# Performance work log

Hardware: AMD Instinct MI355X
Metric: run time of the kernel (lower is better)

The kernel has to match this reference:

```python
import jax, jax.numpy as jnp
import numpy as np

B, C, H, W = 2, 512, 128, 128
L_NUM, HEADS, LEVELS, POINTS = 6, 8, 1, 4
HEAD_DIM = C // HEADS


def setup_inputs() -> dict:
    key = jax.random.key(0)
    ks = jax.random.split(key, 16)
    s = 0.02
    rn = lambda k, shape, scale=s: jax.random.normal(k, shape, jnp.float32) * scale
    return dict(
        bev_feat=jax.random.normal(ks[0], (B, C, H, W), jnp.float32),
        lidar_feat=jax.random.normal(ks[1], (B, C, H, W), jnp.float32),
        Wv=rn(ks[2], (L_NUM, C, C)), bv=jnp.zeros((L_NUM, C), jnp.float32),
        Woff=rn(ks[3], (L_NUM, C, HEADS * LEVELS * POINTS * 2)),
        boff=rn(ks[4], (L_NUM, HEADS * LEVELS * POINTS * 2), 0.5),
        Waw=rn(ks[5], (L_NUM, C, HEADS * LEVELS * POINTS)),
        baw=jnp.zeros((L_NUM, HEADS * LEVELS * POINTS), jnp.float32),
        Wout=rn(ks[6], (L_NUM, C, C)), bout=jnp.zeros((L_NUM, C), jnp.float32),
        ln1_g=jnp.ones((L_NUM, C), jnp.float32), ln1_b=jnp.zeros((L_NUM, C), jnp.float32),
        W1=rn(ks[7], (L_NUM, C, C)), W2=rn(ks[8], (L_NUM, C, C)),
        ln2_g=jnp.ones((L_NUM, C), jnp.float32), ln2_b=jnp.zeros((L_NUM, C), jnp.float32),
        pe_W1=rn(ks[9], (2, C), 0.5),
        pe_bn_g=jnp.ones((C,), jnp.float32), pe_bn_b=jnp.zeros((C,), jnp.float32),
        pe_bn_m=jnp.zeros((C,), jnp.float32), pe_bn_v=jnp.ones((C,), jnp.float32),
        pe_W2=rn(ks[10], (C, C)),
    )


def _layer_norm(x, g, b):
    mu = jnp.mean(x, -1, keepdims=True)
    var = jnp.mean((x - mu) ** 2, -1, keepdims=True)
    return (x - mu) * jax.lax.rsqrt(var + 1e-5) * g + b


def _bilinear_gather(v_flat, locx, locy):
    # v_flat: (B, heads, H*W, d); locx/locy: (B, heads, S) normalized [0,1]
    # grid_sample semantics: align_corners=False, zero padding
    x = locx * W - 0.5
    y = locy * H - 0.5
    x0f = jnp.floor(x); y0f = jnp.floor(y)
    wx = x - x0f; wy = y - y0f
    x0 = x0f.astype(jnp.int32); y0 = y0f.astype(jnp.int32)

    def corner(xi, yi, w):
        inb = (xi >= 0) & (xi < W) & (yi >= 0) & (yi < H)
        idx = jnp.clip(yi, 0, H - 1) * W + jnp.clip(xi, 0, W - 1)
        g = jnp.take_along_axis(v_flat, idx[..., None], axis=2)
        return g * (w * inb)[..., None]

    return (corner(x0, y0, (1 - wx) * (1 - wy)) + corner(x0 + 1, y0, wx * (1 - wy))
            + corner(x0, y0 + 1, (1 - wx) * wy) + corner(x0 + 1, y0 + 1, wx * wy))


def reference(bev_feat, lidar_feat, Wv, bv, Woff, boff, Waw, baw, Wout, bout,
              ln1_g, ln1_b, W1, W2, ln2_g, ln2_b,
              pe_W1, pe_bn_g, pe_bn_b, pe_bn_m, pe_bn_v, pe_W2):
    N = H * W
    # sparse voxelization: keep rows with all-nonzero features, pack valid-first per batch
    lf = jnp.transpose(lidar_feat, (0, 2, 3, 1)).reshape(B, N, C)
    mask = jnp.all(lf != 0, axis=-1)                       # (B,N)
    order = jnp.argsort((~mask).astype(jnp.int32), axis=1, stable=True)  # valid first
    valid = jnp.take_along_axis(mask, order, axis=1)       # (B,N)
    q = jnp.take_along_axis(lf, order[..., None], axis=1) * valid[..., None]
    hh = jnp.arange(N) // W
    ww = jnp.arange(N) % W
    ref_all = jnp.stack([ww / W, hh / H], -1).astype(jnp.float32)  # (N,2) = (x,y)
    ref = jnp.broadcast_to(ref_all, (B, N, 2))
    ref = jnp.take_along_axis(ref, order[..., None], axis=1) * valid[..., None]
    # learned positional embedding (BatchNorm in eval mode)
    pe = ref.reshape(B * N, 2) @ pe_W1
    pe = (pe - pe_bn_m) * jax.lax.rsqrt(pe_bn_v + 1e-5) * pe_bn_g + pe_bn_b
    q_pos = (jax.nn.relu(pe) @ pe_W2).reshape(B, N, C)
    feat_flat = jnp.transpose(bev_feat.reshape(B, C, N), (0, 2, 1))  # (B,N,C)
    norm_xy = jnp.array([W, H], jnp.float32)  # offset normalizer per level (w,h)
    for i in range(L_NUM):
        ident = q
        x = q + q_pos
        v = (feat_flat @ Wv[i] + bv[i]).reshape(B, N, HEADS, HEAD_DIM)
        v_flat = jnp.transpose(v, (0, 2, 1, 3))  # (B,heads,N,d)
        off = (x @ Woff[i] + boff[i]).reshape(B, N, HEADS, LEVELS * POINTS, 2)
        aw = jax.nn.softmax((x @ Waw[i] + baw[i]).reshape(B, N, HEADS, LEVELS * POINTS), axis=-1)
        loc = ref[:, :, None, None, :] + off / norm_xy      # (B,N,heads,P,2)
        locx = jnp.transpose(loc[..., 0], (0, 2, 1, 3)).reshape(B, HEADS, N * POINTS)
        locy = jnp.transpose(loc[..., 1], (0, 2, 1, 3)).reshape(B, HEADS, N * POINTS)
        samp = _bilinear_gather(v_flat, locx, locy).reshape(B, HEADS, N, POINTS, HEAD_DIM)
        awt = jnp.transpose(aw, (0, 2, 1, 3))               # (B,heads,N,P)
        out = jnp.sum(samp * awt[..., None], axis=3)        # (B,heads,N,d)
        out = jnp.transpose(out, (0, 2, 1, 3)).reshape(B, N, C)
        q = out @ Wout[i] + bout[i] + ident                 # dropout in eval = identity
        q = _layer_norm(q, ln1_g[i], ln1_b[i])
        q = jax.nn.relu(q @ W1[i]) @ W2[i] + q
        q = _layer_norm(q, ln2_g[i], ln2_b[i])
    # scatter back to dense (B,C,H,W); invalid voxels stay zero
    slots = jnp.zeros((B, N, C), q.dtype)
    slots = slots.at[jnp.arange(B)[:, None], order].set(q * valid[..., None])
    return jnp.transpose(slots.reshape(B, H, W, C), (0, 3, 1, 2))
```

## Files before the change

### kernel.cpp

```cpp
#include <hip/hip_runtime.h>
#include <cstdint>
#include <cstddef>

#define BDIM 2
#define CDIM 512
#define HDIM 128
#define WDIM 128
#define NDIM (HDIM * WDIM)
#define LNUM 6
#define NHEADS 8
#define HEAD_DIM 64
#define NPTS 4
#define BN_TOT (BDIM * NDIM)

typedef unsigned short u16;
typedef __attribute__((ext_vector_type(8))) short bf16x8;
typedef __attribute__((ext_vector_type(4))) float f32x4;

__device__ __forceinline__ u16 f2bf(float x) {
    unsigned u = __float_as_uint(x);
    u += 0x7fffu + ((u >> 16) & 1u);
    return (u16)(u >> 16);
}
__device__ __forceinline__ float bf2f(u16 h) {
    return __uint_as_float(((unsigned)h) << 16);
}

__device__ __forceinline__ void load_lds16(const void* g, void* l) {
    __builtin_amdgcn_global_load_lds(
        (const __attribute__((address_space(1))) void*)g,
        (__attribute__((address_space(3))) void*)l, 16, 0, 0);
}

__global__ void mask_kernel(const float* __restrict__ lidar, int* __restrict__ mask)
{
    int idx = blockIdx.x * blockDim.x + threadIdx.x;
    if (idx >= BN_TOT) return;
    int b = idx / NDIM;
    int n = idx - b * NDIM;
    const float* p = lidar + (size_t)b * CDIM * NDIM + n;
    int ok = 1;
#pragma unroll 8
    for (int c = 0; c < CDIM; ++c)
        ok &= (p[(size_t)c * NDIM] != 0.0f);
    mask[idx] = ok;
}

__global__ void order_kernel(const int* __restrict__ mask, int* __restrict__ order,
                             int* __restrict__ nvalid)
{
    int b = blockIdx.x;
    const int* m = mask + b * NDIM;
    int* ord = order + b * NDIM;
    __shared__ int part[256];
    __shared__ int totalValid;
    int t = threadIdx.x;
    const int CHUNK = NDIM / 256;
    int base = t * CHUNK;
    int cnt = 0;
    for (int i = 0; i < CHUNK; ++i) cnt += m[base + i];
    part[t] = cnt;
    __syncthreads();
    for (int s = 1; s < 256; s <<= 1) {
        int v = (t >= s) ? part[t - s] : 0;
        __syncthreads();
        part[t] += v;
        __syncthreads();
    }
    if (t == 255) { totalValid = part[255]; nvalid[b] = part[255]; }
    __syncthreads();
    int validBefore = (t == 0) ? 0 : part[t - 1];
    int nv = totalValid;
    for (int i = 0; i < CHUNK; ++i) {
        int n = base + i;
        if (m[n]) { ord[validBefore] = n; validBefore++; }
        else      { int invBefore = n - validBefore; ord[nv + invBefore] = n; }
    }
}

__global__ void ref_kernel(const int* __restrict__ order, const int* __restrict__ nvalid,
                           float* __restrict__ ref)
{
    int idx = blockIdx.x * blockDim.x + threadIdx.x;
    if (idx >= BN_TOT) return;
    int b = idx / NDIM;
    int j = idx - b * NDIM;
    int n = order[idx];
    float flag = (j < nvalid[b]) ? 1.0f : 0.0f;
    int hh = n / WDIM;
    int ww = n - hh * WDIM;
    ref[(size_t)idx * 2 + 0] = ((float)ww / (float)WDIM) * flag;
    ref[(size_t)idx * 2 + 1] = ((float)hh / (float)HDIM) * flag;
}

__global__ void pack_q_kernel(const float* __restrict__ lidar, const int* __restrict__ order,
                              const int* __restrict__ nvalid, u16* __restrict__ q)
{
    __shared__ float tile[32][33];
    __shared__ int ord_s[32];
    int b  = blockIdx.z;
    int j0 = blockIdx.x * 32;
    int c0 = blockIdx.y * 32;
    int tx = threadIdx.x, ty = threadIdx.y;
    if (ty == 0) ord_s[tx] = order[b * NDIM + j0 + tx];
    __syncthreads();
    const float* src = lidar + (size_t)b * CDIM * NDIM;
#pragma unroll
    for (int k = 0; k < 4; ++k) {
        int cl = ty * 4 + k;
        tile[cl][tx] = src[(size_t)(c0 + cl) * NDIM + ord_s[tx]];
    }
    __syncthreads();
    int nv = nvalid[b];
#pragma unroll
    for (int k = 0; k < 4; ++k) {
        int jl = ty * 4 + k;
        int j = j0 + jl;
        float f = (j < nv) ? 1.0f : 0.0f;
        q[((size_t)b * NDIM + j) * CDIM + c0 + tx] = f2bf(tile[tx][jl] * f);
    }
}

__global__ void scatter_kernel(const u16* __restrict__ q, const int* __restrict__ order,
                               const int* __restrict__ nvalid, float* __restrict__ out)
{
    __shared__ float tile[32][33];
    __shared__ int ord_s[32];
    int b  = blockIdx.z;
    int j0 = blockIdx.x * 32;
    int c0 = blockIdx.y * 32;
    int tx = threadIdx.x, ty = threadIdx.y;
    if (ty == 0) ord_s[tx] = order[b * NDIM + j0 + tx];
    __syncthreads();
    int nv = nvalid[b];
#pragma unroll
    for (int k = 0; k < 4; ++k) {
        int jl = ty * 4 + k;
        int j = j0 + jl;
        float f = (j < nv) ? 1.0f : 0.0f;
        tile[jl][tx] = bf2f(q[((size_t)b * NDIM + j) * CDIM + c0 + tx]) * f;
    }
    __syncthreads();
    float* dst = out + (size_t)b * CDIM * NDIM;
#pragma unroll
    for (int k = 0; k < 4; ++k) {
        int cl = ty * 4 + k;
        dst[(size_t)(c0 + cl) * NDIM + ord_s[tx]] = tile[tx][cl];
    }
}

__global__ void tconv_kernel(const float* __restrict__ src, u16* __restrict__ dst)
{
    __shared__ float t[32][33];
    int k0 = blockIdx.x * 32, n0 = blockIdx.y * 32;
    int tx = threadIdx.x, ty = threadIdx.y;
#pragma unroll
    for (int j = 0; j < 4; ++j) {
        int kl = ty * 4 + j;
        t[kl][tx] = src[(size_t)(k0 + kl) * 512 + n0 + tx];
    }
    __syncthreads();
#pragma unroll
    for (int j = 0; j < 4; ++j) {
        int nl = ty * 4 + j;
        dst[(size_t)(n0 + nl) * 512 + k0 + tx] = f2bf(t[tx][nl]);
    }
}

__global__ void tconv_offaw_kernel(const float* __restrict__ woff,
                                   const float* __restrict__ waw,
                                   u16* __restrict__ dst)
{
    __shared__ float t[32][33];
    int k0 = blockIdx.x * 32, n0 = blockIdx.y * 32;
    int tx = threadIdx.x, ty = threadIdx.y;
#pragma unroll
    for (int j = 0; j < 4; ++j) {
        int kl = ty * 4 + j;
        int n = n0 + tx;
        float v = (n < 64) ? woff[(size_t)(k0 + kl) * 64 + n]
                           : waw[(size_t)(k0 + kl) * 32 + (n - 64)];
        t[kl][tx] = v;
    }
    __syncthreads();
#pragma unroll
    for (int j = 0; j < 4; ++j) {
        int nl = ty * 4 + j;
        dst[(size_t)(n0 + nl) * 512 + k0 + tx] = f2bf(t[tx][nl]);
    }
}

__global__ void bev_conv_kernel(const float* __restrict__ bev, u16* __restrict__ dst)
{
    __shared__ float t[32][33];
    int b  = blockIdx.z;
    int n0 = blockIdx.x * 32;
    int c0 = blockIdx.y * 32;
    int tx = threadIdx.x, ty = threadIdx.y;
    const float* src = bev + (size_t)b * CDIM * NDIM;
#pragma unroll
    for (int j = 0; j < 4; ++j) {
        int cl = ty * 4 + j;
        t[cl][tx] = src[(size_t)(c0 + cl) * NDIM + n0 + tx];
    }
    __syncthreads();
#pragma unroll
    for (int j = 0; j < 4; ++j) {
        int nl = ty * 4 + j;
        dst[((size_t)b * NDIM + n0 + nl) * CDIM + c0 + tx] = f2bf(t[tx][nl]);
    }
}

__global__ void pe_hidden_kernel(const float* __restrict__ ref, const float* __restrict__ W1,
                                 const float* __restrict__ g, const float* __restrict__ bb,
                                 const float* __restrict__ m, const float* __restrict__ v,
                                 u16* __restrict__ out)
{
    int row = blockIdx.x;
    float r0 = ref[(size_t)row * 2 + 0];
    float r1 = ref[(size_t)row * 2 + 1];
    for (int c = threadIdx.x; c < CDIM; c += blockDim.x) {
        float pe = r0 * W1[c] + r1 * W1[CDIM + c];
        pe = (pe - m[c]) * rsqrtf(v[c] + 1e-5f) * g[c] + bb[c];
        out[(size_t)row * CDIM + c] = f2bf(fmaxf(pe, 0.0f));
    }
}

__global__ void add_bf_kernel(const u16* __restrict__ q, const u16* __restrict__ qpos,
                              u16* __restrict__ x)
{
    size_t i = (size_t)blockIdx.x * blockDim.x + threadIdx.x;
    uint4 qa = ((const uint4*)q)[i];
    uint4 pv = ((const uint4*)qpos)[i];
    unsigned qw[4] = {qa.x, qa.y, qa.z, qa.w};
    unsigned pw[4] = {pv.x, pv.y, pv.z, pv.w};
    unsigned rw[4];
#pragma unroll
    for (int k = 0; k < 4; ++k) {
        float a0 = bf2f((u16)(qw[k] & 0xffff)), a1 = bf2f((u16)(qw[k] >> 16));
        float p0 = bf2f((u16)(pw[k] & 0xffff)), p1 = bf2f((u16)(pw[k] >> 16));
        rw[k] = (unsigned)f2bf(a0 + p0) | ((unsigned)f2bf(a1 + p1) << 16);
    }
    uint4 r; r.x = rw[0]; r.y = rw[1]; r.z = rw[2]; r.w = rw[3];
    ((uint4*)x)[i] = r;
}

__global__ __launch_bounds__(256) void gemm_bf16(
    const u16* __restrict__ A, const u16* __restrict__ Bt,
    const float* __restrict__ bias, u16* __restrict__ outB, int relu)
{
    __shared__ u16 As[128 * 32];
    __shared__ u16 Bs[128 * 32];
    int tid = threadIdx.x;
    int wave = tid >> 6, lane = tid & 63;
    int wr = wave >> 1, wc = wave & 1;
    int quad = lane >> 4, l15 = lane & 15;
    int bm = blockIdx.y * 128, bn = blockIdx.x * 128;

    f32x4 acc[4][4];
#pragma unroll
    for (int i = 0; i < 4; ++i)
#pragma unroll
        for (int j = 0; j < 4; ++j) { f32x4 z = {0.f, 0.f, 0.f, 0.f}; acc[i][j] = z; }

    int e0 = wave * 512 + lane * 8;
    int e1 = (wave + 4) * 512 + lane * 8;
    const u16* Ag0 = A + (size_t)(bm + (e0 >> 5)) * 512 + (e0 & 31);
    const u16* Ag1 = A + (size_t)(bm + (e1 >> 5)) * 512 + (e1 & 31);
    const u16* Bg0 = Bt + (size_t)(bn + (e0 >> 5)) * 512 + (e0 & 31);
    const u16* Bg1 = Bt + (size_t)(bn + (e1 >> 5)) * 512 + (e1 & 31);

    for (int k0 = 0; k0 < 512; k0 += 32) {
        load_lds16(Ag0 + k0, &As[wave * 512]);
        load_lds16(Ag1 + k0, &As[(wave + 4) * 512]);
        load_lds16(Bg0 + k0, &Bs[wave * 512]);
        load_lds16(Bg1 + k0, &Bs[(wave + 4) * 512]);
        __syncthreads();
        bf16x8 av[4], bv[4];
#pragma unroll
        for (int mi = 0; mi < 4; ++mi)
            av[mi] = *(const bf16x8*)&As[(wr * 64 + mi * 16 + l15) * 32 + quad * 8];
#pragma unroll
        for (int ni = 0; ni < 4; ++ni)
            bv[ni] = *(const bf16x8*)&Bs[(wc * 64 + ni * 16 + l15) * 32 + quad * 8];
#pragma unroll
        for (int mi = 0; mi < 4; ++mi)
#pragma unroll
            for (int ni = 0; ni < 4; ++ni)
                acc[mi][ni] = __builtin_amdgcn_mfma_f32_16x16x32_bf16(
                    av[mi], bv[ni], acc[mi][ni], 0, 0, 0);
        __syncthreads();
    }

    int rowb = bm + wr * 64;
    int colb = bn + wc * 64;
#pragma unroll
    for (int mi = 0; mi < 4; ++mi) {
#pragma unroll
        for (int ni = 0; ni < 4; ++ni) {
            int col = colb + ni * 16 + l15;
            float bi = bias ? bias[col] : 0.0f;
#pragma unroll
            for (int r = 0; r < 4; ++r) {
                int row = rowb + mi * 16 + quad * 4 + r;
                float val = acc[mi][ni][r] + bi;
                if (relu) val = fmaxf(val, 0.0f);
                outB[(size_t)row * 512 + col] = f2bf(val);
            }
        }
    }
}

__global__ __launch_bounds__(512, 4) void gemm_ln(
    const u16* __restrict__ A, const u16* __restrict__ Bt,
    const float* __restrict__ bias, const u16* __restrict__ resid,
    const float* __restrict__ g, const float* __restrict__ bta,
    u16* __restrict__ outQ, const u16* __restrict__ qpos, u16* __restrict__ outX)
{
    __shared__ u16 As[64 * 32];
    __shared__ u16 Bs[512 * 32];
    __shared__ float rs[8][64];
    __shared__ float rq[8][64];
    __shared__ float muL[64], invL[64];

    int tid = threadIdx.x;
    int wv = tid >> 6, lane = tid & 63;
    int quad = lane >> 4, l15 = lane & 15;
    int bm = blockIdx.x * 64;

    f32x4 acc[4][4];
#pragma unroll
    for (int i = 0; i < 4; ++i)
#pragma unroll
        for (int j = 0; j < 4; ++j) { f32x4 z = {0.f, 0.f, 0.f, 0.f}; acc[i][j] = z; }

    const u16* Ag = A + (size_t)(bm + wv * 16 + (lane >> 2)) * 512 + (lane & 3) * 8;
    u16* Al = As + wv * 512;
    const u16* Bg[4];
    u16* Bl[4];
#pragma unroll
    for (int it = 0; it < 4; ++it) {
        int s = wv * 4 + it;
        Bg[it] = Bt + (size_t)(s * 16 + (lane >> 2)) * 512 + (lane & 3) * 8;
        Bl[it] = Bs + s * 512;
    }

    for (int k0 = 0; k0 < 512; k0 += 32) {
        if (wv < 4) load_lds16(Ag + k0, Al);
#pragma unroll
        for (int it = 0; it < 4; ++it) load_lds16(Bg[it] + k0, Bl[it]);
        __syncthreads();
        bf16x8 av[4], bv[4];
#pragma unroll
        for (int mi = 0; mi < 4; ++mi)
            av[mi] = *(const bf16x8*)&As[(mi * 16 + l15) * 32 + quad * 8];
#pragma unroll
        for (int ni = 0; ni < 4; ++ni)
            bv[ni] = *(const bf16x8*)&Bs[(wv * 64 + ni * 16 + l15) * 32 + quad * 8];
#pragma unroll
        for (int mi = 0; mi < 4; ++mi)
#pragma unroll
            for (int ni = 0; ni < 4; ++ni)
                acc[mi][ni] = __builtin_amdgcn_mfma_f32_16x16x32_bf16(
                    av[mi], bv[ni], acc[mi][ni], 0, 0, 0);
        __syncthreads();
    }

    int colb = wv * 64;
    float biasv[4], gv[4], btv[4];
#pragma unroll
    for (int ni = 0; ni < 4; ++ni) {
        int c = colb + ni * 16 + l15;
        biasv[ni] = bias ? bias[c] : 0.0f;
        gv[ni] = g[c];
        btv[ni] = bta[c];
    }
#pragma unroll
    for (int mi = 0; mi < 4; ++mi) {
#pragma unroll
        for (int r = 0; r < 4; ++r) {
            size_t rowoff = (size_t)(bm + mi * 16 + quad * 4 + r) * 512;
#pragma unroll
            for (int ni = 0; ni < 4; ++ni) {
                int col = colb + ni * 16 + l15;
                acc[mi][ni][r] += biasv[ni] + bf2f(resid[rowoff + col]);
            }
        }
    }
#pragma unroll
    for (int mi = 0; mi < 4; ++mi) {
#pragma unroll
        for (int r = 0; r < 4; ++r) {
            float s = acc[mi][0][r] + acc[mi][1][r] + acc[mi][2][r] + acc[mi][3][r];
            float s2 = acc[mi][0][r] * acc[mi][0][r] + acc[mi][1][r] * acc[mi][1][r]
                     + acc[mi][2][r] * acc[mi][2][r] + acc[mi][3][r] * acc[mi][3][r];
#pragma unroll
            for (int m = 1; m < 16; m <<= 1) {
                s  += __shfl_xor(s, m, 64);
                s2 += __shfl_xor(s2, m, 64);
            }
            if (l15 == 0) {
                rs[wv][mi * 16 + quad * 4 + r] = s;
                rq[wv][mi * 16 + quad * 4 + r] = s2;
            }
        }
    }
    __syncthreads();
    if (tid < 64) {
        float s = 0.f, s2 = 0.f;
#pragma unroll
        for (int w = 0; w < 8; ++w) { s += rs[w][tid]; s2 += rq[w][tid]; }
        float mu = s * (1.0f / 512.0f);
        float var = s2 * (1.0f / 512.0f) - mu * mu;
        muL[tid] = mu;
        invL[tid] = rsqrtf(var + 1e-5f);
    }
    __syncthreads();
#pragma unroll
    for (int mi = 0; mi < 4; ++mi) {
#pragma unroll
        for (int r = 0; r < 4; ++r) {
            int lrow = mi * 16 + quad * 4 + r;
            float mu = muL[lrow], iv = invL[lrow];
            size_t rowoff = (size_t)(bm + lrow) * 512;
#pragma unroll
            for (int ni = 0; ni < 4; ++ni) {
                int col = colb + ni * 16 + l15;
                float y = (acc[mi][ni][r] - mu) * iv * gv[ni] + btv[ni];
                outQ[rowoff + col] = f2bf(y);
                if (outX)
                    outX[rowoff + col] = f2bf(y + bf2f(qpos[rowoff + col]));
            }
        }
    }
}

__global__ __launch_bounds__(256) void gemm_offaw(
    const u16* __restrict__ A, const u16* __restrict__ Bt,
    const float* __restrict__ boff, const float* __restrict__ baw,
    u16* __restrict__ offb, u16* __restrict__ awb)
{
    __shared__ u16 As[128 * 32];
    __shared__ u16 Bs[128 * 32];
    int tid = threadIdx.x;
    int wave = tid >> 6, lane = tid & 63;
    int wr = wave >> 1, wc = wave & 1;
    int quad = lane >> 4, l15 = lane & 15;
    int bm = blockIdx.y * 128;

    f32x4 acc[4][4];
#pragma unroll
    for (int i = 0; i < 4; ++i)
#pragma unroll
        for (int j = 0; j < 4; ++j) { f32x4 z = {0.f, 0.f, 0.f, 0.f}; acc[i][j] = z; }

    int e0 = wave * 512 + lane * 8;
    int e1 = (wave + 4) * 512 + lane * 8;
    int br0 = e0 >> 5; if (br0 > 95) br0 = 95;
    int br1 = e1 >> 5; if (br1 > 95) br1 = 95;
    const u16* Ag0 = A + (size_t)(bm + (e0 >> 5)) * 512 + (e0 & 31);
    const u16* Ag1 = A + (size_t)(bm + (e1 >> 5)) * 512 + (e1 & 31);
    const u16* Bg0 = Bt + (size_t)br0 * 512 + (e0 & 31);
    const u16* Bg1 = Bt + (size_t)br1 * 512 + (e1 & 31);

    for (int k0 = 0; k0 < 512; k0 += 32) {
        load_lds16(Ag0 + k0, &As[wave * 512]);
        load_lds16(Ag1 + k0, &As[(wave + 4) * 512]);
        load_lds16(Bg0 + k0, &Bs[wave * 512]);
        load_lds16(Bg1 + k0, &Bs[(wave + 4) * 512]);
        __syncthreads();
        bf16x8 av[4], bv[4];
#pragma unroll
        for (int mi = 0; mi < 4; ++mi)
            av[mi] = *(const bf16x8*)&As[(wr * 64 + mi * 16 + l15) * 32 + quad * 8];
#pragma unroll
        for (int ni = 0; ni < 4; ++ni)
            bv[ni] = *(const bf16x8*)&Bs[(wc * 64 + ni * 16 + l15) * 32 + quad * 8];
#pragma unroll
        for (int mi = 0; mi < 4; ++mi)
#pragma unroll
            for (int ni = 0; ni < 4; ++ni)
                acc[mi][ni] = __builtin_amdgcn_mfma_f32_16x16x32_bf16(
                    av[mi], bv[ni], acc[mi][ni], 0, 0, 0);
        __syncthreads();
    }

    int rowb = bm + wr * 64;
#pragma unroll
    for (int mi = 0; mi < 4; ++mi) {
#pragma unroll
        for (int ni = 0; ni < 4; ++ni) {
            int col = wc * 64 + ni * 16 + l15;
            if (col < 96) {
                float bi = (col < 64) ? boff[col] : baw[col - 64];
#pragma unroll
                for (int r = 0; r < 4; ++r) {
                    int row = rowb + mi * 16 + quad * 4 + r;
                    float val = acc[mi][ni][r] + bi;
                    if (col < 64) offb[(size_t)row * 64 + col] = f2bf(val);
                    else          awb[(size_t)row * 32 + (col - 64)] = f2bf(val);
                }
            }
        }
    }
}

__global__ __launch_bounds__(256) void sample_kernel(
    const float* __restrict__ ref, const u16* __restrict__ off,
    const u16* __restrict__ aw, const u16* __restrict__ v,
    u16* __restrict__ out)
{
    int bj = blockIdx.x * 4 + (threadIdx.x >> 6);
    int lane = threadIdx.x & 63;
    int h  = lane >> 3;
    int d8 = (lane & 7) * 8;
    int b  = bj >> 14;

    float rx = ref[(size_t)bj * 2 + 0];
    float ry = ref[(size_t)bj * 2 + 1];
    uint4 offv = *(const uint4*)(off + (size_t)bj * 64 + h * 8);
    uint2 awv  = *(const uint2*)(aw + (size_t)bj * 32 + h * 4);

    float l0 = bf2f((u16)(awv.x & 0xffff)), l1 = bf2f((u16)(awv.x >> 16));
    float l2 = bf2f((u16)(awv.y & 0xffff)), l3 = bf2f((u16)(awv.y >> 16));
    float mx = fmaxf(fmaxf(l0, l1), fmaxf(l2, l3));
    float e[4];
    e[0] = expf(l0 - mx); e[1] = expf(l1 - mx);
    e[2] = expf(l2 - mx); e[3] = expf(l3 - mx);
    float inv_es = 1.0f / (e[0] + e[1] + e[2] + e[3]);

    const u16* vb = v + (size_t)b * NDIM * CDIM + h * HEAD_DIM + d8;
    float acc[8] = {0.f, 0.f, 0.f, 0.f, 0.f, 0.f, 0.f, 0.f};
    unsigned ow[4] = {offv.x, offv.y, offv.z, offv.w};

#pragma unroll
    for (int p = 0; p < NPTS; ++p) {
        float ox = bf2f((u16)(ow[p] & 0xffff));
        float oy = bf2f((u16)(ow[p] >> 16));
        float X = rx * (float)WDIM + ox - 0.5f;
        float Y = ry * (float)HDIM + oy - 0.5f;
        float x0f = floorf(X), y0f = floorf(Y);
        float wx = X - x0f, wy = Y - y0f;
        int x0 = (int)x0f, y0 = (int)y0f;
        float ep = e[p];
#pragma unroll
        for (int cy = 0; cy < 2; ++cy) {
            int yy = y0 + cy;
            float wyc = cy ? wy : (1.0f - wy);
            int yin = (yy >= 0) & (yy < HDIM);
            int yc = min(max(yy, 0), HDIM - 1);
#pragma unroll
            for (int cx = 0; cx < 2; ++cx) {
                int xx = x0 + cx;
                float wxc = cx ? wx : (1.0f - wx);
                int xin = (xx >= 0) & (xx < WDIM);
                int xc = min(max(xx, 0), WDIM - 1);
                float wgt = ep * wyc * wxc * (float)(yin & xin);
                uint4 vv = *(const uint4*)(vb + (size_t)(yc * WDIM + xc) * CDIM);
                acc[0] += wgt * bf2f((u16)(vv.x & 0xffff));
                acc[1] += wgt * bf2f((u16)(vv.x >> 16));
                acc[2] += wgt * bf2f((u16)(vv.y & 0xffff));
                acc[3] += wgt * bf2f((u16)(vv.y >> 16));
                acc[4] += wgt * bf2f((u16)(vv.z & 0xffff));
                acc[5] += wgt * bf2f((u16)(vv.z >> 16));
                acc[6] += wgt * bf2f((u16)(vv.w & 0xffff));
                acc[7] += wgt * bf2f((u16)(vv.w >> 16));
            }
        }
    }
    uint4 r;
    r.x = (unsigned)f2bf(acc[0] * inv_es) | ((unsigned)f2bf(acc[1] * inv_es) << 16);
    r.y = (unsigned)f2bf(acc[2] * inv_es) | ((unsigned)f2bf(acc[3] * inv_es) << 16);
    r.z = (unsigned)f2bf(acc[4] * inv_es) | ((unsigned)f2bf(acc[5] * inv_es) << 16);
    r.w = (unsigned)f2bf(acc[6] * inv_es) | ((unsigned)f2bf(acc[7] * inv_es) << 16);
    *(uint4*)(out + (size_t)bj * CDIM + h * HEAD_DIM + d8) = r;
}

extern "C" void kernel_launch(void* const* d_in, const int* in_sizes, int n_in,
                              void* d_out, int out_size, void* d_ws, size_t ws_size,
                              hipStream_t stream)
{
    const float* bev   = (const float*)d_in[0];
    const float* lidar = (const float*)d_in[1];
    const float* Wv    = (const float*)d_in[2];
    const float* bv    = (const float*)d_in[3];
    const float* Woff  = (const float*)d_in[4];
    const float* boff  = (const float*)d_in[5];
    const float* Waw   = (const float*)d_in[6];
    const float* baw   = (const float*)d_in[7];
    const float* Wout  = (const float*)d_in[8];
    const float* bout  = (const float*)d_in[9];
    const float* ln1g  = (const float*)d_in[10];
    const float* ln1b  = (const float*)d_in[11];
    const float* W1    = (const float*)d_in[12];
    const float* W2    = (const float*)d_in[13];
    const float* ln2g  = (const float*)d_in[14];
    const float* ln2b  = (const float*)d_in[15];
    const float* peW1  = (const float*)d_in[16];
    const float* peg   = (const float*)d_in[17];
    const float* peb   = (const float*)d_in[18];
    const float* pem   = (const float*)d_in[19];
    const float* pev   = (const float*)d_in[20];
    const float* pevW2 = (const float*)d_in[21];

    const size_t NC = (size_t)BN_TOT * CDIM;

    char* base = (char*)d_ws;
    u16* q      = (u16*)base;
    u16* actX   = (u16*)(base + NC * 2);
    u16* actA   = (u16*)(base + NC * 4);
    u16* actB   = (u16*)(base + NC * 6);
    u16* wt     = (u16*)(base + NC * 8);
    u16* offawt = wt + 4 * 512 * 512;
    u16* offb   = offawt + 96 * 512;
    u16* awb    = offb + (size_t)BN_TOT * 64;
    float* refb = (float*)(awb + (size_t)BN_TOT * 32);
    int* mask   = (int*)(refb + (size_t)BN_TOT * 2);
    int* order  = mask + BN_TOT;
    int* nvalid = order + BN_TOT;

    u16* qpos_bf = (u16*)d_out;
    u16* featT   = (u16*)d_out + NC;

    dim3 blk328(32, 8);
    dim3 gemm_grid(4, 256);
    dim3 offaw_grid(1, 256);
    int  ln_grid = BN_TOT / 64;

    mask_kernel<<<BN_TOT / 256, 256, 0, stream>>>(lidar, mask);
    order_kernel<<<BDIM, 256, 0, stream>>>(mask, order, nvalid);
    ref_kernel<<<BN_TOT / 256, 256, 0, stream>>>(order, nvalid, refb);
    pack_q_kernel<<<dim3(NDIM / 32, CDIM / 32, BDIM), blk328, 0, stream>>>(lidar, order, nvalid, q);
    bev_conv_kernel<<<dim3(NDIM / 32, CDIM / 32, BDIM), blk328, 0, stream>>>(bev, featT);

    pe_hidden_kernel<<<BN_TOT, 128, 0, stream>>>(refb, peW1, peg, peb, pem, pev, actA);
    tconv_kernel<<<dim3(16, 16), blk328, 0, stream>>>(pevW2, wt);
    gemm_bf16<<<gemm_grid, 256, 0, stream>>>(actA, wt, nullptr, qpos_bf, 0);

    add_bf_kernel<<<(unsigned)(NC / 8 / 256), 256, 0, stream>>>(q, qpos_bf, actX);

    for (int i = 0; i < LNUM; ++i) {
        const size_t WO = (size_t)i * CDIM * CDIM;
        tconv_kernel<<<dim3(16, 16), blk328, 0, stream>>>(Wv + WO,   wt + 0 * 262144);
        tconv_kernel<<<dim3(16, 16), blk328, 0, stream>>>(Wout + WO, wt + 1 * 262144);
        tconv_kernel<<<dim3(16, 16), blk328, 0, stream>>>(W1 + WO,   wt + 2 * 262144);
        tconv_kernel<<<dim3(16, 16), blk328, 0, stream>>>(W2 + WO,   wt + 3 * 262144);
        tconv_offaw_kernel<<<dim3(16, 3), blk328, 0, stream>>>(
            Woff + (size_t)i * CDIM * 64, Waw + (size_t)i * CDIM * 32, offawt);

        gemm_offaw<<<offaw_grid, 256, 0, stream>>>(actX, offawt,
                                                   boff + i * 64, baw + i * 32, offb, awb);
        gemm_bf16<<<gemm_grid, 256, 0, stream>>>(featT, wt + 0 * 262144, bv + i * CDIM,
                                                 actA, 0);
        sample_kernel<<<BN_TOT / 4, 256, 0, stream>>>(refb, offb, awb, actA, actB);
        gemm_ln<<<ln_grid, 512, 0, stream>>>(actB, wt + 1 * 262144, bout + i * CDIM,
                                             q, ln1g + i * CDIM, ln1b + i * CDIM,
                                             q, nullptr, nullptr);
        gemm_bf16<<<gemm_grid, 256, 0, stream>>>(q, wt + 2 * 262144, nullptr, actA, 1);
        gemm_ln<<<ln_grid, 512, 0, stream>>>(actA, wt + 3 * 262144, nullptr,
                                             q, ln2g + i * CDIM, ln2b + i * CDIM,
                                             q, qpos_bf,
                                             (i < LNUM - 1) ? actX : nullptr);
    }

    scatter_kernel<<<dim3(NDIM / 32, CDIM / 32, BDIM), blk328, 0, stream>>>(
        q, order, nvalid, (float*)d_out);
}
```

Before: 1.959 ms.

## Double-buffer LDS in GEMMs and batch weight transposes up front

Gives the three GEMM kernels double-buffered LDS tiles, so the load of the next K-slice is issued before computing on the current one, with one barrier per iteration instead of two. All per-layer weight transpose/convert launches are replaced by a few batched launches (grid z over layers) before the loop, storing every layer's bf16 weights separately. The actX buffer is dropped and actB reused for x. This hides global-load latency and removes about 30 small launches, at the cost of doubled LDS use per block, which can lower occupancy in gemm_ln.

```diff
diff --git a/kernel.cpp b/kernel.cpp
--- a/kernel.cpp
+++ b/kernel.cpp
@@ -149,9 +149,12 @@
     }
 }
 
-__global__ void tconv_kernel(const float* __restrict__ src, u16* __restrict__ dst)
+__global__ void tconv_b_kernel(const float* __restrict__ src0, u16* __restrict__ dst0)
 {
     __shared__ float t[32][33];
+    int z = blockIdx.z;
+    const float* src = src0 + (size_t)z * 512 * 512;
+    u16* dst = dst0 + (size_t)z * 512 * 512;
     int k0 = blockIdx.x * 32, n0 = blockIdx.y * 32;
     int tx = threadIdx.x, ty = threadIdx.y;
 #pragma unroll
@@ -167,11 +170,15 @@
     }
 }
 
-__global__ void tconv_offaw_kernel(const float* __restrict__ woff,
-                                   const float* __restrict__ waw,
-                                   u16* __restrict__ dst)
+__global__ void tconv_offaw_b_kernel(const float* __restrict__ woff0,
+                                     const float* __restrict__ waw0,
+                                     u16* __restrict__ dst0)
 {
     __shared__ float t[32][33];
+    int z = blockIdx.z;
+    const float* woff = woff0 + (size_t)z * 512 * 64;
+    const float* waw  = waw0 + (size_t)z * 512 * 32;
+    u16* dst = dst0 + (size_t)z * 96 * 512;
     int k0 = blockIdx.x * 32, n0 = blockIdx.y * 32;
     int tx = threadIdx.x, ty = threadIdx.y;
 #pragma unroll
@@ -249,8 +256,8 @@
     const u16* __restrict__ A, const u16* __restrict__ Bt,
     const float* __restrict__ bias, u16* __restrict__ outB, int relu)
 {
-    __shared__ u16 As[128 * 32];
-    __shared__ u16 Bs[128 * 32];
+    __shared__ u16 As[2][128 * 32];
+    __shared__ u16 Bs[2][128 * 32];
     int tid = threadIdx.x;
     int wave = tid >> 6, lane = tid & 63;
     int wr = wave >> 1, wc = wave & 1;
@@ -270,26 +277,34 @@
     const u16* Bg0 = Bt + (size_t)(bn + (e0 >> 5)) * 512 + (e0 & 31);
     const u16* Bg1 = Bt + (size_t)(bn + (e1 >> 5)) * 512 + (e1 & 31);
 
-    for (int k0 = 0; k0 < 512; k0 += 32) {
-        load_lds16(Ag0 + k0, &As[wave * 512]);
-        load_lds16(Ag1 + k0, &As[(wave + 4) * 512]);
-        load_lds16(Bg0 + k0, &Bs[wave * 512]);
-        load_lds16(Bg1 + k0, &Bs[(wave + 4) * 512]);
+    load_lds16(Ag0, &As[0][wave * 512]);
+    load_lds16(Ag1, &As[0][(wave + 4) * 512]);
+    load_lds16(Bg0, &Bs[0][wave * 512]);
+    load_lds16(Bg1, &Bs[0][(wave + 4) * 512]);
+
+    for (int it = 0; it < 16; ++it) {
         __syncthreads();
+        int cur = it & 1, nxt = cur ^ 1;
+        if (it < 15) {
+            int kn = (it + 1) * 32;
+            load_lds16(Ag0 + kn, &As[nxt][wave * 512]);
+            load_lds16(Ag1 + kn, &As[nxt][(wave + 4) * 512]);
+            load_lds16(Bg0 + kn, &Bs[nxt][wave * 512]);
+            load_lds16(Bg1 + kn, &Bs[nxt][(wave + 4) * 512]);
+        }
         bf16x8 av[4], bv[4];
 #pragma unroll
         for (int mi = 0; mi < 4; ++mi)
-            av[mi] = *(const bf16x8*)&As[(wr * 64 + mi * 16 + l15) * 32 + quad * 8];
+            av[mi] = *(const bf16x8*)&As[cur][(wr * 64 + mi * 16 + l15) * 32 + quad * 8];
 #pragma unroll
         for (int ni = 0; ni < 4; ++ni)
-            bv[ni] = *(const bf16x8*)&Bs[(wc * 64 + ni * 16 + l15) * 32 + quad * 8];
+            bv[ni] = *(const bf16x8*)&Bs[cur][(wc * 64 + ni * 16 + l15) * 32 + quad * 8];
 #pragma unroll
         for (int mi = 0; mi < 4; ++mi)
 #pragma unroll
             for (int ni = 0; ni < 4; ++ni)
                 acc[mi][ni] = __builtin_amdgcn_mfma_f32_16x16x32_bf16(
                     av[mi], bv[ni], acc[mi][ni], 0, 0, 0);
-        __syncthreads();
     }
 
     int rowb = bm + wr * 64;
@@ -317,8 +332,8 @@
     const float* __restrict__ g, const float* __restrict__ bta,
     u16* __restrict__ outQ, const u16* __restrict__ qpos, u16* __restrict__ outX)
 {
-    __shared__ u16 As[64 * 32];
-    __shared__ u16 Bs[512 * 32];
+    __shared__ u16 As[2][64 * 32];
+    __shared__ u16 Bs[2][512 * 32];
     __shared__ float rs[8][64];
     __shared__ float rq[8][64];
     __shared__ float muL[64], invL[64];
@@ -335,35 +350,40 @@
         for (int j = 0; j < 4; ++j) { f32x4 z = {0.f, 0.f, 0.f, 0.f}; acc[i][j] = z; }
 
     const u16* Ag = A + (size_t)(bm + wv * 16 + (lane >> 2)) * 512 + (lane & 3) * 8;
-    u16* Al = As + wv * 512;
     const u16* Bg[4];
-    u16* Bl[4];
 #pragma unroll
     for (int it = 0; it < 4; ++it) {
         int s = wv * 4 + it;
         Bg[it] = Bt + (size_t)(s * 16 + (lane >> 2)) * 512 + (lane & 3) * 8;
-        Bl[it] = Bs + s * 512;
-    }
-
-    for (int k0 = 0; k0 < 512; k0 += 32) {
-        if (wv < 4) load_lds16(Ag + k0, Al);
-#pragma unroll
-        for (int it = 0; it < 4; ++it) load_lds16(Bg[it] + k0, Bl[it]);
+    }
+
+    if (wv < 4) load_lds16(Ag, &As[0][wv * 512]);
+#pragma unroll
+    for (int it = 0; it < 4; ++it) load_lds16(Bg[it], &Bs[0][(wv * 4 + it) * 512]);
+
+    for (int kk = 0; kk < 16; ++kk) {
         __syncthreads();
+        int cur = kk & 1, nxt = cur ^ 1;
+        if (kk < 15) {
+            int kn = (kk + 1) * 32;
+            if (wv < 4) load_lds16(Ag + kn, &As[nxt][wv * 512]);
+#pragma unroll
+            for (int it = 0; it < 4; ++it)
+                load_lds16(Bg[it] + kn, &Bs[nxt][(wv * 4 + it) * 512]);
+        }
         bf16x8 av[4], bv[4];
 #pragma unroll
         for (int mi = 0; mi < 4; ++mi)
-            av[mi] = *(const bf16x8*)&As[(mi * 16 + l15) * 32 + quad * 8];
+            av[mi] = *(const bf16x8*)&As[cur][(mi * 16 + l15) * 32 + quad * 8];
 #pragma unroll
         for (int ni = 0; ni < 4; ++ni)
-            bv[ni] = *(const bf16x8*)&Bs[(wv * 64 + ni * 16 + l15) * 32 + quad * 8];
+            bv[ni] = *(const bf16x8*)&Bs[cur][(wv * 64 + ni * 16 + l15) * 32 + quad * 8];
 #pragma unroll
         for (int mi = 0; mi < 4; ++mi)
 #pragma unroll
             for (int ni = 0; ni < 4; ++ni)
                 acc[mi][ni] = __builtin_amdgcn_mfma_f32_16x16x32_bf16(
                     av[mi], bv[ni], acc[mi][ni], 0, 0, 0);
-        __syncthreads();
     }
 
     int colb = wv * 64;
@@ -440,8 +460,8 @@
     const float* __restrict__ boff, const float* __restrict__ baw,
     u16* __restrict__ offb, u16* __restrict__ awb)
 {
-    __shared__ u16 As[128 * 32];
-    __shared__ u16 Bs[128 * 32];
+    __shared__ u16 As[2][128 * 32];
+    __shared__ u16 Bs[2][128 * 32];
     int tid = threadIdx.x;
     int wave = tid >> 6, lane = tid & 63;
     int wr = wave >> 1, wc = wave & 1;
@@ -463,26 +483,34 @@
     const u16* Bg0 = Bt + (size_t)br0 * 512 + (e0 & 31);
     const u16* Bg1 = Bt + (size_t)br1 * 512 + (e1 & 31);
 
-    for (int k0 = 0; k0 < 512; k0 += 32) {
-        load_lds16(Ag0 + k0, &As[wave * 512]);
-        load_lds16(Ag1 + k0, &As[(wave + 4) * 512]);
-        load_lds16(Bg0 + k0, &Bs[wave * 512]);
-        load_lds16(Bg1 + k0, &Bs[(wave + 4) * 512]);
+    load_lds16(Ag0, &As[0][wave * 512]);
+    load_lds16(Ag1, &As[0][(wave + 4) * 512]);
+    load_lds16(Bg0, &Bs[0][wave * 512]);
+    load_lds16(Bg1, &Bs[0][(wave + 4) * 512]);
+
+    for (int it = 0; it < 16; ++it) {
         __syncthreads();
+        int cur = it & 1, nxt = cur ^ 1;
+        if (it < 15) {
+            int kn = (it + 1) * 32;
+            load_lds16(Ag0 + kn, &As[nxt][wave * 512]);
+            load_lds16(Ag1 + kn, &As[nxt][(wave + 4) * 512]);
+            load_lds16(Bg0 + kn, &Bs[nxt][wave * 512]);
+            load_lds16(Bg1 + kn, &Bs[nxt][(wave + 4) * 512]);
+        }
         bf16x8 av[4], bv[4];
 #pragma unroll
         for (int mi = 0; mi < 4; ++mi)
-            av[mi] = *(const bf16x8*)&As[(wr * 64 + mi * 16 + l15) * 32 + quad * 8];
+            av[mi] = *(const bf16x8*)&As[cur][(wr * 64 + mi * 16 + l15) * 32 + quad * 8];
 #pragma unroll
         for (int ni = 0; ni < 4; ++ni)
-            bv[ni] = *(const bf16x8*)&Bs[(wc * 64 + ni * 16 + l15) * 32 + quad * 8];
+            bv[ni] = *(const bf16x8*)&Bs[cur][(wc * 64 + ni * 16 + l15) * 32 + quad * 8];
 #pragma unroll
         for (int mi = 0; mi < 4; ++mi)
 #pragma unroll
             for (int ni = 0; ni < 4; ++ni)
                 acc[mi][ni] = __builtin_amdgcn_mfma_f32_16x16x32_bf16(
                     av[mi], bv[ni], acc[mi][ni], 0, 0, 0);
-        __syncthreads();
     }
 
     int rowb = bm + wr * 64;
@@ -601,18 +629,23 @@
     const float* peb   = (const float*)d_in[18];
     const float* pem   = (const float*)d_in[19];
     const float* pev   = (const float*)d_in[20];
-    const float* pevW2 = (const float*)d_in[21];
+    const float* peW2  = (const float*)d_in[21];
 
     const size_t NC = (size_t)BN_TOT * CDIM;
+    const size_t WSZ = 512 * 512;
 
     char* base = (char*)d_ws;
     u16* q      = (u16*)base;
-    u16* actX   = (u16*)(base + NC * 2);
-    u16* actA   = (u16*)(base + NC * 4);
-    u16* actB   = (u16*)(base + NC * 6);
-    u16* wt     = (u16*)(base + NC * 8);
-    u16* offawt = wt + 4 * 512 * 512;
-    u16* offb   = offawt + 96 * 512;
+    u16* actA   = (u16*)(base + NC * 2);
+    u16* actB   = (u16*)(base + NC * 4);
+    u16* wt     = (u16*)(base + NC * 6);
+    u16* wtv    = wt;
+    u16* wtout  = wt + 6 * WSZ;
+    u16* wt1    = wt + 12 * WSZ;
+    u16* wt2    = wt + 18 * WSZ;
+    u16* wtpe   = wt + 24 * WSZ;
+    u16* offawt = wt + 25 * WSZ;
+    u16* offb   = offawt + 6 * 96 * 512;
     u16* awb    = offb + (size_t)BN_TOT * 64;
     float* refb = (float*)(awb + (size_t)BN_TOT * 32);
     int* mask   = (int*)(refb + (size_t)BN_TOT * 2);
@@ -633,34 +666,32 @@
     pack_q_kernel<<<dim3(NDIM / 32, CDIM / 32, BDIM), blk328, 0, stream>>>(lidar, order, nvalid, q);
     bev_conv_kernel<<<dim3(NDIM / 32, CDIM / 32, BDIM), blk328, 0, stream>>>(bev, featT);
 
+    tconv_b_kernel<<<dim3(16, 16, 6), blk328, 0, stream>>>(Wv,   wtv);
+    tconv_b_kernel<<<dim3(16, 16, 6), blk328, 0, stream>>>(Wout, wtout);
+    tconv_b_kernel<<<dim3(16, 16, 6), blk328, 0, stream>>>(W1,   wt1);
+    tconv_b_kernel<<<dim3(16, 16, 6), blk328, 0, stream>>>(W2,   wt2);
+    tconv_b_kernel<<<dim3(16, 16, 1), blk328, 0, stream>>>(peW2, wtpe);
+    tconv_offaw_b_kernel<<<dim3(16, 3, 6), blk328, 0, stream>>>(Woff, Waw, offawt);
+
     pe_hidden_kernel<<<BN_TOT, 128, 0, stream>>>(refb, peW1, peg, peb, pem, pev, actA);
-    tconv_kernel<<<dim3(16, 16), blk328, 0, stream>>>(pevW2, wt);
-    gemm_bf16<<<gemm_grid, 256, 0, stream>>>(actA, wt, nullptr, qpos_bf, 0);
-
-    add_bf_kernel<<<(unsigned)(NC / 8 / 256), 256, 0, stream>>>(q, qpos_bf, actX);
+    gemm_bf16<<<gemm_grid, 256, 0, stream>>>(actA, wtpe, nullptr, qpos_bf, 0);
+
+    add_bf_kernel<<<(unsigned)(NC / 8 / 256), 256, 0, stream>>>(q, qpos_bf, actB);
 
     for (int i = 0; i < LNUM; ++i) {
-        const size_t WO = (size_t)i * CDIM * CDIM;
-        tconv_kernel<<<dim3(16, 16), blk328, 0, stream>>>(Wv + WO,   wt + 0 * 262144);
-        tconv_kernel<<<dim3(16, 16), blk328, 0, stream>>>(Wout + WO, wt + 1 * 262144);
-        tconv_kernel<<<dim3(16, 16), blk328, 0, stream>>>(W1 + WO,   wt + 2 * 262144);
-        tconv_kernel<<<dim3(16, 16), blk328, 0, stream>>>(W2 + WO,   wt + 3 * 262144);
-        tconv_offaw_kernel<<<dim3(16, 3), blk328, 0, stream>>>(
-            Woff + (size_t)i * CDIM * 64, Waw + (size_t)i * CDIM * 32, offawt);
-
-        gemm_offaw<<<offaw_grid, 256, 0, stream>>>(actX, offawt,
+        gemm_offaw<<<offaw_grid, 256, 0, stream>>>(actB, offawt + (size_t)i * 96 * 512,
                                                    boff + i * 64, baw + i * 32, offb, awb);
-        gemm_bf16<<<gemm_grid, 256, 0, stream>>>(featT, wt + 0 * 262144, bv + i * CDIM,
-                                                 actA, 0);
+        gemm_bf16<<<gemm_grid, 256, 0, stream>>>(featT, wtv + (size_t)i * WSZ,
+                                                 bv + i * CDIM, actA, 0);
         sample_kernel<<<BN_TOT / 4, 256, 0, stream>>>(refb, offb, awb, actA, actB);
-        gemm_ln<<<ln_grid, 512, 0, stream>>>(actB, wt + 1 * 262144, bout + i * CDIM,
+        gemm_ln<<<ln_grid, 512, 0, stream>>>(actB, wtout + (size_t)i * WSZ, bout + i * CDIM,
                                              q, ln1g + i * CDIM, ln1b + i * CDIM,
                                              q, nullptr, nullptr);
-        gemm_bf16<<<gemm_grid, 256, 0, stream>>>(q, wt + 2 * 262144, nullptr, actA, 1);
-        gemm_ln<<<ln_grid, 512, 0, stream>>>(actA, wt + 3 * 262144, nullptr,
+        gemm_bf16<<<gemm_grid, 256, 0, stream>>>(q, wt1 + (size_t)i * WSZ, nullptr, actA, 1);
+        gemm_ln<<<ln_grid, 512, 0, stream>>>(actA, wt2 + (size_t)i * WSZ, nullptr,
                                              q, ln2g + i * CDIM, ln2b + i * CDIM,
                                              q, qpos_bf,
-                                             (i < LNUM - 1) ? actX : nullptr);
+                                             (i < LNUM - 1) ? actB : nullptr);
     }
 
     scatter_kernel<<<dim3(NDIM / 32, CDIM / 32, BDIM), blk328, 0, stream>>>(
```

New measurement: 1.835 ms. -6.3%, faster.
